# Kernel optimization log

Hardware: AMD Instinct MI355X
Metric: run time of the kernel (lower is better)

The kernel has to match this reference:

```python
import jax, jax.numpy as jnp
import numpy as np

EPS = 1e-7
B, N, DIM, NH, HD, WIN, HASH_WIN = 2, 1024, 512, 8, 64, 64, 8


def expmap0(v, c):
    sqrt_c = jnp.clip(jnp.sqrt(c), EPS)
    v_norm = jnp.linalg.norm(v, axis=-1, keepdims=True)
    is_zero = v_norm < EPS
    safe = jnp.clip(v_norm, EPS)
    mag = jnp.tanh(sqrt_c * safe) / sqrt_c
    return jnp.where(is_zero, jnp.zeros_like(v), mag * (v / safe))


def poincare_dist(x, y, c):
    # x: (B,H,N,1,D), y: (B,H,N,W,D), c: (B,1,1,1,1) -> (B,H,N,W)
    sqrt_c = jnp.clip(jnp.sqrt(c), EPS)
    x2 = jnp.sum(x * x, -1, keepdims=True)
    y2 = jnp.sum(y * y, -1, keepdims=True)
    xy = jnp.sum(x * y, -1, keepdims=True)
    num = (1 - 2 * c * xy + c * y2) * x + (1 - c * x2) * (-y)
    den = 1 - 2 * c * xy + c * c * x2 * y2
    diff = num / jnp.clip(den, EPS)
    dn = jnp.linalg.norm(diff, axis=-1)
    arg = jnp.minimum(jnp.squeeze(sqrt_c, -1) * jnp.clip(dn, EPS), 1.0 - EPS)
    return 2.0 * jnp.arctanh(arg) / jnp.squeeze(sqrt_c, -1)


def sliding_windows(t, w):
    # t: (B,H,N,D) -> (B,H,N,w,D), left-padded causal window
    Bb, H, Nn, D = t.shape
    pad = jnp.zeros((Bb, H, w - 1, D), t.dtype)
    tp = jnp.concatenate([pad, t], axis=2)
    idx = jnp.arange(w)[None, :] + jnp.arange(Nn)[:, None]  # (N,w)
    return tp[:, :, idx, :]


def layernorm(x, s, b):
    m = jnp.mean(x, -1, keepdims=True)
    v = jnp.var(x, -1, keepdims=True)
    return (x - m) / jnp.sqrt(v + 1e-6) * s + b


def rope(x, cos, sin):
    # x: (B,N,H,hd), cos/sin: (N, hd//2) -- complex rotation in real arithmetic
    xr, xi = jnp.split(x, 2, axis=-1)
    cos = cos[None, :, None, :]
    sin = sin[None, :, None, :]
    return jnp.concatenate([xr * cos - xi * sin, xr * sin + xi * cos], axis=-1)


def setup_inputs() -> dict:
    key = jax.random.key(0)
    ks = jax.random.split(key, 10)
    x = jax.random.normal(ks[0], (B, N, DIM), jnp.float32)
    pos = jnp.arange(N, dtype=jnp.float32)
    inv = 1.0 / (10000.0 ** (jnp.arange(0, HD, 2, dtype=jnp.float32) / HD))
    ang = pos[:, None] * inv[None, :]  # (N, HD//2)
    freqs_cos, freqs_sin = jnp.cos(ang), jnp.sin(ang)
    c = jax.random.uniform(ks[1], (B,), jnp.float32) * 0.9 + 0.1
    s = 0.02
    Wq = jax.random.normal(ks[2], (DIM, DIM), jnp.float32) * s
    Wk = jax.random.normal(ks[3], (DIM, DIM), jnp.float32) * s
    Wv = jax.random.normal(ks[4], (DIM, DIM), jnp.float32) * s
    Wo = jax.random.normal(ks[5], (DIM, DIM), jnp.float32) * s
    W1 = jax.random.normal(ks[6], (DIM, 4 * DIM), jnp.float32) * s
    W2 = jax.random.normal(ks[7], (4 * DIM, DIM), jnp.float32) * s
    bq = jnp.zeros((DIM,)); bk = jnp.zeros((DIM,)); bv = jnp.zeros((DIM,))
    bo = jnp.zeros((DIM,)); b1 = jnp.zeros((4 * DIM,)); b2 = jnp.zeros((DIM,))
    ln1_s = jnp.ones((DIM,)); ln1_b = jnp.zeros((DIM,))
    ln2_s = jnp.ones((DIM,)); ln2_b = jnp.zeros((DIM,))
    geo_scale = jnp.ones((NH, 1, 1), jnp.float32)
    hash_offset = jax.random.normal(ks[8], (1, 1, NH, HD), jnp.float32) * 0.01
    return dict(x=x, freqs_cos=freqs_cos, freqs_sin=freqs_sin, c=c,
                Wq=Wq, bq=bq, Wk=Wk, bk=bk, Wv=Wv, bv=bv, Wo=Wo, bo=bo,
                W1=W1, b1=b1, W2=W2, b2=b2,
                ln1_s=ln1_s, ln1_b=ln1_b, ln2_s=ln2_s, ln2_b=ln2_b,
                geo_scale=geo_scale, hash_offset=hash_offset)


def reference(x, freqs_cos, freqs_sin, c, Wq, bq, Wk, bk, Wv, bv, Wo, bo,
              W1, b1, W2, b2, ln1_s, ln1_b, ln2_s, ln2_b, geo_scale, hash_offset):
    x_res = x
    xn = layernorm(x, ln1_s, ln1_b)
    q = (xn @ Wq + bq).reshape(B, N, NH, HD)
    k = (xn @ Wk + bk).reshape(B, N, NH, HD)
    v = (xn @ Wv + bv).reshape(B, N, NH, HD)
    q = q + hash_offset * jnp.log(1.0 + HASH_WIN)
    q_rot = rope(q, freqs_cos, freqs_sin)
    k_rot = rope(k, freqs_cos, freqs_sin)
    c_b = c.reshape(B, 1, 1, 1)
    q_h = expmap0(q_rot, c_b)
    k_h = expmap0(k_rot, c_b)
    q_h, k_h, v = (t.transpose(0, 2, 1, 3) for t in (q_h, k_h, v))  # (B,H,N,D)
    k_win = sliding_windows(k_h, WIN)  # (B,H,N,W,D)
    v_win = sliding_windows(v, WIN)
    dist = poincare_dist(q_h[:, :, :, None, :], k_win, c.reshape(B, 1, 1, 1, 1))  # (B,H,N,W)
    scores = -geo_scale * dist
    w = jax.nn.softmax(scores, axis=-1)
    attn = jnp.einsum('bhnw,bhnwd->bhnd', w, v_win)
    attn = attn.transpose(0, 2, 1, 3).reshape(B, N, DIM)
    x_out = x_res + (attn @ Wo + bo)
    h = layernorm(x_out, ln2_s, ln2_b)
    ffn = jax.nn.gelu(h @ W1 + b1) @ W2 + b2
    return x_out + ffn
```

## Files before the change

### kernel.cpp

```cpp
#include <hip/hip_runtime.h>
#include <math.h>
#include <stdint.h>

#define Bn   2
#define Nn   1024
#define DIMn 512
#define NHn  8
#define HDn  64
#define QKVS 1536
#define EPSF 1e-7f

typedef __attribute__((ext_vector_type(8))) short short8;
typedef __attribute__((ext_vector_type(4))) float floatx4;
typedef __attribute__((ext_vector_type(4))) float fx4;
typedef __attribute__((ext_vector_type(4))) unsigned short usx4;

__device__ __forceinline__ unsigned short f2bf(float f) {
  union { float f; uint32_t u; } v; v.f = f;
  uint32_t u = v.u;
  return (unsigned short)((u + 0x7FFFu + ((u >> 16) & 1u)) >> 16);
}
__device__ __forceinline__ float bf2f(unsigned short h) {
  union { uint32_t u; float f; } v; v.u = ((uint32_t)h) << 16;
  return v.f;
}

__device__ __forceinline__ float wsum(float v) {
#pragma unroll
  for (int m = 32; m >= 1; m >>= 1) v += __shfl_xor(v, m, 64);
  return v;
}

__device__ __forceinline__ float gelu_tanh(float x) {
  const float k0 = 0.7978845608028654f;
  float x3 = x * x * x;
  return 0.5f * x * (1.f + tanhf(k0 * (x + 0.044715f * x3)));
}

__device__ __forceinline__ void glds16(const unsigned short* g, unsigned short* l) {
  __builtin_amdgcn_global_load_lds((const __attribute__((address_space(1))) void*)g,
                                   (__attribute__((address_space(3))) void*)l, 16, 0, 0);
}

__device__ void tr64(const float* __restrict__ W, unsigned short* __restrict__ hi,
                     unsigned short* __restrict__ lo, int K, int N, int tix, int tid,
                     float* tile ) {
  int ntn = N >> 6;
  int kt = tix / ntn, nt = tix - kt * ntn;
  int k0 = kt * 64, n0 = nt * 64;
  int rb = tid >> 4, c4 = (tid & 15) * 4;
#pragma unroll
  for (int rr = 0; rr < 4; ++rr) {
    int r = rr * 16 + rb;
    fx4 v = *(const fx4*)&W[(size_t)(k0 + r) * N + n0 + c4];
    tile[r * 65 + c4] = v.x;
    tile[r * 65 + c4 + 1] = v.y;
    tile[r * 65 + c4 + 2] = v.z;
    tile[r * 65 + c4 + 3] = v.w;
  }
  __syncthreads();
#pragma unroll
  for (int rr = 0; rr < 4; ++rr) {
    int r = rr * 16 + rb;
    usx4 hv, lv;
#pragma unroll
    for (int j = 0; j < 4; ++j) {
      float v = tile[(c4 + j) * 65 + r];
      unsigned short h = f2bf(v);
      hv[j] = h;
      lv[j] = f2bf(v - bf2f(h));
    }
    size_t oi = (size_t)(n0 + r) * K + k0 + c4;
    *(usx4*)&hi[oi] = hv;
    if (lo) *(usx4*)&lo[oi] = lv;
  }
  __syncthreads();
}

__global__ __launch_bounds__(256) void prep_kernel(
    const float* __restrict__ Wq, const float* __restrict__ Wk,
    const float* __restrict__ Wv,
    unsigned short* __restrict__ Wcat_hi, unsigned short* __restrict__ Wcat_lo,
    const float* __restrict__ bq, const float* __restrict__ bk,
    const float* __restrict__ bv, float* __restrict__ bias_cat,
    const float* __restrict__ x, const float* __restrict__ ln1s,
    const float* __restrict__ ln1b,
    unsigned short* __restrict__ xn_hi, unsigned short* __restrict__ xn_lo) {
  __shared__ float tile[64 * 65];
  __shared__ float red[2][4];
  int bid = blockIdx.x;
  int tid = threadIdx.x;
  if (bid < 64) {
    tr64(Wq, Wcat_hi, Wcat_lo, 512, 512, bid, tid, tile);
    return;
  }
  if (bid < 128) {
    tr64(Wk, Wcat_hi + 512 * 512, Wcat_lo + 512 * 512, 512, 512, bid - 64, tid, tile);
    return;
  }
  if (bid < 192) {
    tr64(Wv, Wcat_hi + 1024 * 512, nullptr, 512, 512, bid - 128, tid, tile);
    return;
  }
  if (bid == 192) {
    for (int i = tid; i < 512; i += 256) {
      bias_cat[i] = bq[i];
      bias_cat[512 + i] = bk[i];
      bias_cat[1024 + i] = bv[i];
    }
    return;
  }
  int row = bid - 193;
  const float* xr = x + (size_t)row * DIMn;
  float2 xv = *(const float2*)(xr + tid * 2);
  float s  = xv.x + xv.y;
  float s2 = xv.x * xv.x + xv.y * xv.y;
  s = wsum(s); s2 = wsum(s2);
  int wv = tid >> 6;
  if ((tid & 63) == 0) { red[0][wv] = s; red[1][wv] = s2; }
  __syncthreads();
  s  = red[0][0] + red[0][1] + red[0][2] + red[0][3];
  s2 = red[1][0] + red[1][1] + red[1][2] + red[1][3];
  float mean = s * (1.f / DIMn);
  float var  = s2 * (1.f / DIMn) - mean * mean;
  float rstd = rsqrtf(var + 1e-6f);
  int d = tid * 2;
  float2 gv = *(const float2*)(ln1s + d);
  float2 bv2 = *(const float2*)(ln1b + d);
  float o0 = (xv.x - mean) * rstd * gv.x + bv2.x;
  float o1 = (xv.y - mean) * rstd * gv.y + bv2.y;
  size_t idx = (size_t)row * DIMn + d;
  unsigned short h0 = f2bf(o0), h1 = f2bf(o1);
  ushort2 hv; hv.x = h0; hv.y = h1;
  *(ushort2*)(xn_hi + idx) = hv;
  ushort2 lv; lv.x = f2bf(o0 - bf2f(h0)); lv.y = f2bf(o1 - bf2f(h1));
  *(ushort2*)(xn_lo + idx) = lv;
}

__global__ __launch_bounds__(256) void ln_kernel(const float* __restrict__ x,
                                                 const float* __restrict__ g,
                                                 const float* __restrict__ be,
                                                 unsigned short* __restrict__ yhi) {
  __shared__ float red[2][4];
  int row = blockIdx.x;
  int tid = threadIdx.x;
  const float* xr = x + (size_t)row * DIMn;
  float2 xv = *(const float2*)(xr + tid * 2);
  float s  = xv.x + xv.y;
  float s2 = xv.x * xv.x + xv.y * xv.y;
  s = wsum(s); s2 = wsum(s2);
  int wv = tid >> 6;
  if ((tid & 63) == 0) { red[0][wv] = s; red[1][wv] = s2; }
  __syncthreads();
  s  = red[0][0] + red[0][1] + red[0][2] + red[0][3];
  s2 = red[1][0] + red[1][1] + red[1][2] + red[1][3];
  float mean = s * (1.f / DIMn);
  float var  = s2 * (1.f / DIMn) - mean * mean;
  float rstd = rsqrtf(var + 1e-6f);
  int d = tid * 2;
  float2 gv = *(const float2*)(g + d);
  float2 bv = *(const float2*)(be + d);
  float o0 = (xv.x - mean) * rstd * gv.x + bv.x;
  float o1 = (xv.y - mean) * rstd * gv.y + bv.y;
  size_t idx = (size_t)row * DIMn + d;
  ushort2 hv; hv.x = f2bf(o0); hv.y = f2bf(o1);
  *(ushort2*)(yhi + idx) = hv;
}

template <int BM, int BN, int BKT, int EPI, int OUTBF16>
__global__ __launch_bounds__(256) void gemm_db(
    const unsigned short* __restrict__ Ahi,
    const unsigned short* __restrict__ Bhi,
    const float* __restrict__ bias, const float* __restrict__ res,
    void* __restrict__ outp, int M, int N, int K) {
  constexpr int FI = BM / 32, FJ = BN / 32;
  constexpr int AE = BM * BKT, BE = BN * BKT;
  constexpr int CPR = BKT / 8;
  constexpr int ACH = BM * CPR, BCH = BN * CPR;
  constexpr int CST = BN + 4;
  constexpr int STG = AE + BE;
  constexpr int SMEM_EPI = BM * CST * 2;
  constexpr int SMEM_N = (2 * STG > SMEM_EPI) ? 2 * STG : SMEM_EPI;
  __shared__ __align__(16) unsigned short smem[SMEM_N];

  int tid = threadIdx.x;
  int lane = tid & 63;
  int wid = tid >> 6;
  int wm = (wid >> 1) * (BM / 2), wn = (wid & 1) * (BN / 2);
  int bm = blockIdx.y * BM, bn = blockIdx.x * BN;
  int m16 = lane & 15, kg = lane >> 4;

  floatx4 acc[FI][FJ];
#pragma unroll
  for (int i = 0; i < FI; ++i)
#pragma unroll
    for (int j = 0; j < FJ; ++j) { floatx4 z = {0.f, 0.f, 0.f, 0.f}; acc[i][j] = z; }

  const unsigned short* aph = Ahi + (size_t)bm * K;
  const unsigned short* bph = Bhi + (size_t)bn * K;

  auto stage = [&](int k0, unsigned short* As, unsigned short* Bs) {
    for (int c = tid; c < ACH; c += 256) {
      int row = c / CPR, ci = c % CPR;
      int sci = ci ^ (row & 7);
      glds16(aph + (size_t)row * K + k0 + sci * 8, As + c * 8);
    }
    for (int c = tid; c < BCH; c += 256) {
      int row = c / CPR, ci = c % CPR;
      int sci = ci ^ (row & 7);
      glds16(bph + (size_t)row * K + k0 + sci * 8, Bs + c * 8);
    }
  };

  const int NT = K / BKT;
  stage(0, smem, smem + AE);
  __syncthreads();
  int cur = 0;
  for (int t = 0; t < NT; ++t) {
    unsigned short* As = smem + cur * STG;
    unsigned short* Bs = As + AE;
    int nxt = cur ^ 1;
    if (t + 1 < NT) stage((t + 1) * BKT, smem + nxt * STG, smem + nxt * STG + AE);
#pragma unroll
    for (int ks = 0; ks < BKT / 32; ++ks) {
      short8 ah[FI], bh[FJ];
#pragma unroll
      for (int i = 0; i < FI; ++i) {
        int r = wm + i * 16 + m16;
        ah[i] = *(const short8*)&As[r * BKT + (((ks * 4 + kg) ^ (r & 7)) << 3)];
      }
#pragma unroll
      for (int j = 0; j < FJ; ++j) {
        int r = wn + j * 16 + m16;
        bh[j] = *(const short8*)&Bs[r * BKT + (((ks * 4 + kg) ^ (r & 7)) << 3)];
      }
#pragma unroll
      for (int i = 0; i < FI; ++i)
#pragma unroll
        for (int j = 0; j < FJ; ++j)
          acc[i][j] = __builtin_amdgcn_mfma_f32_16x16x32_bf16(ah[i], bh[j], acc[i][j], 0, 0, 0);
    }
    __syncthreads();
    cur = nxt;
  }

  float* Cs = (float*)smem;
#pragma unroll
  for (int i = 0; i < FI; ++i)
#pragma unroll
    for (int j = 0; j < FJ; ++j)
#pragma unroll
      for (int r = 0; r < 4; ++r)
        Cs[(wm + i * 16 + kg * 4 + r) * CST + wn + j * 16 + m16] = acc[i][j][r];
  __syncthreads();
  constexpr int TOT = BM * BN / 4;
  for (int t = tid; t < TOT; t += 256) {
    int row = (t << 2) / BN;
    int col = (t << 2) & (BN - 1);
    fx4 v = *(const fx4*)&Cs[row * CST + col];
    fx4 bs = *(const fx4*)&bias[bn + col];
    v = v + bs;
    size_t gidx = (size_t)(bm + row) * N + bn + col;
    if constexpr (EPI == 1) {
      fx4 rr = *(const fx4*)&res[gidx];
      v = v + rr;
    }
    if constexpr (EPI == 2) {
      v.x = gelu_tanh(v.x); v.y = gelu_tanh(v.y);
      v.z = gelu_tanh(v.z); v.w = gelu_tanh(v.w);
    }
    if constexpr (OUTBF16) {
      usx4 h;
      h.x = f2bf(v.x); h.y = f2bf(v.y); h.z = f2bf(v.z); h.w = f2bf(v.w);
      *(usx4*)((unsigned short*)outp + gidx) = h;
    } else {
      *(fx4*)((float*)outp + gidx) = v;
    }
  }
}

__global__ __launch_bounds__(256) void qkv_gemm(
    const unsigned short* __restrict__ Ahi, const unsigned short* __restrict__ Alo,
    const unsigned short* __restrict__ Bhi, const unsigned short* __restrict__ Blo,
    const float* __restrict__ bias, float* __restrict__ outp,
    const float* __restrict__ Wo, const float* __restrict__ W1,
    const float* __restrict__ W2,
    unsigned short* __restrict__ Wo_t, unsigned short* __restrict__ W1_t,
    unsigned short* __restrict__ W2_t) {
  constexpr int BM = 64, BN = 64, BKT = 32, K = 512, N = QKVS;
  constexpr int FI = 2, FJ = 2;
  constexpr int AE = BM * BKT, BE = BN * BKT;
  constexpr int CST = BN + 4;
  constexpr int STG = 2 * (AE + BE);
  constexpr int SMEM_EPI = BM * CST * 2;
  constexpr int SMEM_N = (2 * STG > SMEM_EPI) ? 2 * STG : SMEM_EPI;
  __shared__ __align__(16) unsigned short smem[SMEM_N];

  int tid = threadIdx.x;
  int bid = blockIdx.x;

  if (bid >= 768) {
    float* tile = (float*)smem;
    int tix = bid - 768;
    if (tix < 64)       tr64(Wo, Wo_t, nullptr, 512, 512, tix, tid, tile);
    else if (tix < 320) tr64(W1, W1_t, nullptr, 512, 2048, tix - 64, tid, tile);
    else                tr64(W2, W2_t, nullptr, 2048, 512, tix - 320, tid, tile);
    return;
  }

  int lane = tid & 63;
  int wid = tid >> 6;
  int wm = (wid >> 1) * 32, wn = (wid & 1) * 32;
  int bm = (bid / 24) * BM, bn = (bid % 24) * BN;
  int m16 = lane & 15, kg = lane >> 4;
  bool dos = bn < 1024;

  floatx4 acc[FI][FJ];
#pragma unroll
  for (int i = 0; i < FI; ++i)
#pragma unroll
    for (int j = 0; j < FJ; ++j) { floatx4 z = {0.f, 0.f, 0.f, 0.f}; acc[i][j] = z; }

  const unsigned short* aph = Ahi + (size_t)bm * K;
  const unsigned short* bph = Bhi + (size_t)bn * K;
  const unsigned short* apl = Alo + (size_t)bm * K;
  const unsigned short* bpl = Blo + (size_t)bn * K;

  auto stage = [&](int k0, unsigned short* buf) {
    {
      int c = tid;
      int row = c >> 2, ci = c & 3;
      int sci = ci ^ ((row >> 1) & 3);
      glds16(aph + (size_t)row * K + k0 + sci * 8, buf + c * 8);
      if (dos) glds16(apl + (size_t)row * K + k0 + sci * 8, buf + AE + c * 8);
    }
    {
      int c = tid;
      int row = c >> 2, ci = c & 3;
      int sci = ci ^ ((row >> 1) & 3);
      glds16(bph + (size_t)row * K + k0 + sci * 8, buf + 2 * AE + c * 8);
      if (dos) glds16(bpl + (size_t)row * K + k0 + sci * 8, buf + 2 * AE + BE + c * 8);
    }
  };

  const int NT = K / BKT;
  stage(0, smem);
  __syncthreads();
  int cur = 0;
  for (int t = 0; t < NT; ++t) {
    unsigned short* buf = smem + cur * STG;
    unsigned short* AsHi = buf;
    unsigned short* AsLo = buf + AE;
    unsigned short* BsHi = buf + 2 * AE;
    unsigned short* BsLo = buf + 2 * AE + BE;
    int nxt = cur ^ 1;
    if (t + 1 < NT) stage((t + 1) * BKT, smem + nxt * STG);

    short8 ah[FI], bh[FJ], al[FI], bl[FJ];
#pragma unroll
    for (int i = 0; i < FI; ++i) {
      int r = wm + i * 16 + m16;
      int off = r * BKT + ((kg ^ ((r >> 1) & 3)) << 3);
      ah[i] = *(const short8*)&AsHi[off];
      if (dos) al[i] = *(const short8*)&AsLo[off];
    }
#pragma unroll
    for (int j = 0; j < FJ; ++j) {
      int r = wn + j * 16 + m16;
      int off = r * BKT + ((kg ^ ((r >> 1) & 3)) << 3);
      bh[j] = *(const short8*)&BsHi[off];
      if (dos) bl[j] = *(const short8*)&BsLo[off];
    }
#pragma unroll
    for (int i = 0; i < FI; ++i)
#pragma unroll
      for (int j = 0; j < FJ; ++j) {
        acc[i][j] = __builtin_amdgcn_mfma_f32_16x16x32_bf16(ah[i], bh[j], acc[i][j], 0, 0, 0);
        if (dos) {
          acc[i][j] = __builtin_amdgcn_mfma_f32_16x16x32_bf16(al[i], bh[j], acc[i][j], 0, 0, 0);
          acc[i][j] = __builtin_amdgcn_mfma_f32_16x16x32_bf16(ah[i], bl[j], acc[i][j], 0, 0, 0);
        }
      }
    __syncthreads();
    cur = nxt;
  }

  float* Cs = (float*)smem;
#pragma unroll
  for (int i = 0; i < FI; ++i)
#pragma unroll
    for (int j = 0; j < FJ; ++j)
#pragma unroll
      for (int r = 0; r < 4; ++r)
        Cs[(wm + i * 16 + kg * 4 + r) * CST + wn + j * 16 + m16] = acc[i][j][r];
  __syncthreads();
  constexpr int TOT = BM * BN / 4;
  for (int t = tid; t < TOT; t += 256) {
    int row = (t << 2) / BN;
    int col = (t << 2) & (BN - 1);
    fx4 v = *(const fx4*)&Cs[row * CST + col];
    fx4 bs = *(const fx4*)&bias[bn + col];
    v = v + bs;
    size_t gidx = (size_t)(bm + row) * N + bn + col;
    *(fx4*)(outp + gidx) = v;
  }
}

__global__ __launch_bounds__(512) void attn_fused(const float* __restrict__ qkv,
                                                  const float* __restrict__ fcos,
                                                  const float* __restrict__ fsin,
                                                  const float* __restrict__ cvec,
                                                  const float* __restrict__ geo,
                                                  const float* __restrict__ hash,
                                                  unsigned short* __restrict__ attn_out) {
  __shared__ unsigned short Qhi[32][72], Qlo[32][72];
  __shared__ unsigned short Khi[96][72], Klo[96][72];
  __shared__ unsigned short Vt[64][104];
  __shared__ unsigned short Pb[32][104];
  __shared__ float Sf[32][97];
  __shared__ float x2s[32], bxs[32], y2s[96], gys[96];

  int tid = threadIdx.x, lane = tid & 63, wv = tid >> 6;
  int bid = blockIdx.x;
  int nt = bid & 31, h = (bid >> 5) & 7, b = bid >> 8;
  int n0 = nt * 32;
  float c = cvec[b];
  float sqc = sqrtf(c);
  float rsqc = 1.f / sqc;
  float gs = geo[h];
  int dr = lane & 31;
  bool hih = lane >= 32;
  const float LOG9 = 2.1972245773362196f;
  float hofr = hash[h * HDn + dr] * LOG9;
  float hofi = hash[h * HDn + dr + 32] * LOG9;

  for (int i = tid; i < 32 * 52; i += 512) ((uint32_t*)Pb)[i] = 0u;

#pragma unroll
  for (int i = 0; i < 4; ++i) {
    int q = wv * 4 + i;
    int n = n0 + q;
    size_t bas = (size_t)(b * Nn + n) * QKVS + h * HDn;
    float qr = qkv[bas + dr] + hofr;
    float qi = qkv[bas + dr + 32] + hofi;
    float cs = fcos[n * 32 + dr], sn = fsin[n * 32 + dr];
    float qv = hih ? (qr * sn + qi * cs) : (qr * cs - qi * sn);
    float nq = sqrtf(wsum(qv * qv));
    float sq = fmaxf(nq, EPSF);
    float t = sqc * sq;
    float em = expf(-2.f * t);
    float opem = 1.f + em;
    float mag = ((1.f - em) / opem) * rsqc;
    float sech2 = 4.f * em / (opem * opem);
    float oq = (nq < EPSF) ? 0.f : mag * (qv / sq);
    unsigned short hh = f2bf(oq);
    Qhi[q][lane] = hh;
    Qlo[q][lane] = f2bf(oq - bf2f(hh));
    if (lane == 0) {
      x2s[q] = (nq < EPSF) ? 0.f : mag * mag;
      bxs[q] = (nq < EPSF) ? 1.f : sech2;
    }
  }
#pragma unroll 4
  for (int i = 0; i < 12; ++i) {
    int r = wv * 12 + i;
    int gi = n0 - 64 + r;
    float ok = 0.f, vf = 0.f, y2 = 0.f, gy = 1.f;
    if (gi >= 0) {
      size_t bas = (size_t)(b * Nn + gi) * QKVS + h * HDn;
      float kr = qkv[bas + 512 + dr];
      float ki = qkv[bas + 512 + dr + 32];
      vf = qkv[bas + 1024 + lane];
      float cs = fcos[gi * 32 + dr], sn = fsin[gi * 32 + dr];
      float kv = hih ? (kr * sn + ki * cs) : (kr * cs - ki * sn);
      float nk = sqrtf(wsum(kv * kv));
      float sk = fmaxf(nk, EPSF);
      float t = sqc * sk;
      float em = expf(-2.f * t);
      float opem = 1.f + em;
      float mag = ((1.f - em) / opem) * rsqc;
      float sech2 = 4.f * em / (opem * opem);
      ok = (nk < EPSF) ? 0.f : mag * (kv / sk);
      y2 = (nk < EPSF) ? 0.f : mag * mag;
      gy = (nk < EPSF) ? 1.f : sech2;
    }
    unsigned short hh = f2bf(ok);
    Khi[r][lane] = hh;
    Klo[r][lane] = f2bf(ok - bf2f(hh));
    Vt[lane][r] = f2bf(vf);
    if (lane == 0) { y2s[r] = y2; gys[r] = gy; }
  }
  __syncthreads();

  int m16 = lane & 15, kg = lane >> 4;
#pragma unroll
  for (int uu = 0; uu < 2; ++uu) {
    int u = wv + uu * 8;
    if (u < 12) {
      int mt = u / 6, ntile = u % 6;
      floatx4 acc = {0.f, 0.f, 0.f, 0.f};
#pragma unroll
      for (int ks = 0; ks < 2; ++ks) {
        short8 ah = *(const short8*)&Qhi[mt * 16 + m16][ks * 32 + kg * 8];
        short8 al = *(const short8*)&Qlo[mt * 16 + m16][ks * 32 + kg * 8];
        short8 bh = *(const short8*)&Khi[ntile * 16 + m16][ks * 32 + kg * 8];
        short8 bl = *(const short8*)&Klo[ntile * 16 + m16][ks * 32 + kg * 8];
        acc = __builtin_amdgcn_mfma_f32_16x16x32_bf16(ah, bh, acc, 0, 0, 0);
        acc = __builtin_amdgcn_mfma_f32_16x16x32_bf16(al, bh, acc, 0, 0, 0);
        acc = __builtin_amdgcn_mfma_f32_16x16x32_bf16(ah, bl, acc, 0, 0, 0);
      }
#pragma unroll
      for (int r = 0; r < 4; ++r) Sf[mt * 16 + kg * 4 + r][ntile * 16 + m16] = acc[r];
    }
  }
  __syncthreads();

#pragma unroll
  for (int i = 0; i < 4; ++i) {
    int nl = wv * 4 + i;
    int r = nl + 1 + lane;
    float xy = Sf[nl][r];
    float x2 = x2s[nl], y2 = y2s[r];
    float bx = bxs[nl], gy = gys[r];

    float den = fmaf(c * c * x2, y2, fmaf(-2.f * c, xy, 1.f));
    den = fmaxf(den, EPSF);
    float rden = 1.f / den;
    float s2 = fmaxf(x2 - 2.f * xy + y2, 0.f);
    float z = sqrtf(c * s2 * rden);
    float omz2 = bx * gy * rden;
    float opz = 1.f + fminf(z, 1.f);
    float ratio = fminf(opz * opz / omz2, 1.9999999e7f);
    float sc = -gs * logf(ratio) * rsqc;

    float e = expf(sc);
    float se = wsum(e);
    Pb[nl][r] = f2bf(e / se);
  }
  __syncthreads();

  {
    int mt = wv >> 2, ntile = wv & 3;
    floatx4 acc = {0.f, 0.f, 0.f, 0.f};
#pragma unroll
    for (int ks = 0; ks < 3; ++ks) {
      short8 a = *(const short8*)&Pb[mt * 16 + m16][ks * 32 + kg * 8];
      short8 bb = *(const short8*)&Vt[ntile * 16 + m16][ks * 32 + kg * 8];
      acc = __builtin_amdgcn_mfma_f32_16x16x32_bf16(a, bb, acc, 0, 0, 0);
    }
#pragma unroll
    for (int r = 0; r < 4; ++r) {
      int qrow = mt * 16 + kg * 4 + r;
      int d = ntile * 16 + m16;
      attn_out[(size_t)(b * Nn + n0 + qrow) * DIMn + h * HDn + d] = f2bf(acc[r]);
    }
  }
}

extern "C" void kernel_launch(void* const* d_in, const int* in_sizes, int n_in,
                              void* d_out, int out_size, void* d_ws, size_t ws_size,
                              hipStream_t stream) {
  const float* x    = (const float*)d_in[0];
  const float* fcos = (const float*)d_in[1];
  const float* fsin = (const float*)d_in[2];
  const float* cvec = (const float*)d_in[3];
  const float* Wq = (const float*)d_in[4];  const float* bq = (const float*)d_in[5];
  const float* Wk = (const float*)d_in[6];  const float* bk = (const float*)d_in[7];
  const float* Wv = (const float*)d_in[8];  const float* bv = (const float*)d_in[9];
  const float* Wo = (const float*)d_in[10]; const float* bo = (const float*)d_in[11];
  const float* W1 = (const float*)d_in[12]; const float* b1 = (const float*)d_in[13];
  const float* W2 = (const float*)d_in[14]; const float* b2 = (const float*)d_in[15];
  const float* ln1s = (const float*)d_in[16]; const float* ln1b = (const float*)d_in[17];
  const float* ln2s = (const float*)d_in[18]; const float* ln2b = (const float*)d_in[19];
  const float* geo  = (const float*)d_in[20]; const float* hash = (const float*)d_in[21];
  float* out = (float*)d_out;
  char* base = (char*)d_ws;

  unsigned short* Wcat_hi = (unsigned short*)(base + 0);
  unsigned short* Wcat_lo = (unsigned short*)(base + 1572864);
  unsigned short* Wo_t    = (unsigned short*)(base + 3145728);
  unsigned short* W1_t    = (unsigned short*)(base + 3670016);
  unsigned short* W2_t    = (unsigned short*)(base + 5767168);
  unsigned short* xn_hi   = (unsigned short*)(base + 7864320);
  unsigned short* xn_lo   = (unsigned short*)(base + 9961472);
  float*          qkv     = (float*)(base + 12058624);
  unsigned short* attnb   = (unsigned short*)(base + 7864320);
  float*          xout    = (float*)(base + 9961472);
  unsigned short* hbuf    = (unsigned short*)(base + 14155776);
  unsigned short* mid     = (unsigned short*)(base + 16252928);
  float*          bias_cat= (float*)(base + 24641536);

  const int M = Bn * Nn;

  prep_kernel<<<193 + M, 256, 0, stream>>>(Wq, Wk, Wv, Wcat_hi, Wcat_lo,
                                           bq, bk, bv, bias_cat,
                                           x, ln1s, ln1b, xn_hi, xn_lo);
  qkv_gemm<<<768 + 576, 256, 0, stream>>>(
      xn_hi, xn_lo, Wcat_hi, Wcat_lo, bias_cat, qkv,
      Wo, W1, W2, Wo_t, W1_t, W2_t);
  attn_fused<<<Bn * NHn * (Nn / 32), 512, 0, stream>>>(qkv, fcos, fsin, cvec, geo, hash, attnb);
  gemm_db<32, 32, 64, 1, 0><<<dim3(DIMn / 32, M / 32), 256, 0, stream>>>(
      attnb, Wo_t, bo, x, xout, M, DIMn, 512);
  ln_kernel<<<M, 256, 0, stream>>>(xout, ln2s, ln2b, hbuf);
  gemm_db<64, 64, 64, 2, 1><<<dim3(2048 / 64, M / 64), 256, 0, stream>>>(
      hbuf, W1_t, b1, nullptr, mid, M, 2048, 512);
  gemm_db<32, 32, 64, 1, 0><<<dim3(DIMn / 32, M / 32), 256, 0, stream>>>(
      mid, W2_t, b2, xout, out, M, DIMn, 2048);
}
```

Before: 179.9 us.

## Precompute hyperbolic Q/K transform in separate kernel to avoid redundant window recomputation

Moves the RoPE, hash offset, expmap0 and bf16 hi/lo split of Q and K, plus the V bf16 conversion, into a new per-token kernel that writes to workspace buffers. The attention kernel then only loads the precomputed bf16 tiles and auxiliary norms. This removes the 3x recomputation of the K transform caused by overlapping 96-row windows per 32-query tile. In exchange it adds a kernel launch and an extra global write/read round trip of the transformed tensors.

```diff
diff --git a/kernel.cpp b/kernel.cpp
--- a/kernel.cpp
+++ b/kernel.cpp
@@ -406,44 +406,31 @@
   }
 }
 
-__global__ __launch_bounds__(512) void attn_fused(const float* __restrict__ qkv,
-                                                  const float* __restrict__ fcos,
-                                                  const float* __restrict__ fsin,
-                                                  const float* __restrict__ cvec,
-                                                  const float* __restrict__ geo,
-                                                  const float* __restrict__ hash,
-                                                  unsigned short* __restrict__ attn_out) {
-  __shared__ unsigned short Qhi[32][72], Qlo[32][72];
-  __shared__ unsigned short Khi[96][72], Klo[96][72];
-  __shared__ unsigned short Vt[64][104];
-  __shared__ unsigned short Pb[32][104];
-  __shared__ float Sf[32][97];
-  __shared__ float x2s[32], bxs[32], y2s[96], gys[96];
-
-  int tid = threadIdx.x, lane = tid & 63, wv = tid >> 6;
-  int bid = blockIdx.x;
-  int nt = bid & 31, h = (bid >> 5) & 7, b = bid >> 8;
-  int n0 = nt * 32;
+__global__ __launch_bounds__(512) void qk_transform(
+    const float* __restrict__ qkv, const float* __restrict__ fcos,
+    const float* __restrict__ fsin, const float* __restrict__ cvec,
+    const float* __restrict__ hash,
+    unsigned short* __restrict__ qh_hi, unsigned short* __restrict__ qh_lo,
+    unsigned short* __restrict__ kh_hi, unsigned short* __restrict__ kh_lo,
+    unsigned short* __restrict__ vb, float2* __restrict__ qaux,
+    float2* __restrict__ kaux) {
+  int tid = threadIdx.x, lane = tid & 63, h = tid >> 6;
+  int token = blockIdx.x;
+  int b = token >> 10, n = token & 1023;
   float c = cvec[b];
-  float sqc = sqrtf(c);
-  float rsqc = 1.f / sqc;
-  float gs = geo[h];
+  float sqc = sqrtf(c), rsqc = 1.f / sqc;
   int dr = lane & 31;
   bool hih = lane >= 32;
   const float LOG9 = 2.1972245773362196f;
-  float hofr = hash[h * HDn + dr] * LOG9;
-  float hofi = hash[h * HDn + dr + 32] * LOG9;
-
-  for (int i = tid; i < 32 * 52; i += 512) ((uint32_t*)Pb)[i] = 0u;
-
-#pragma unroll
-  for (int i = 0; i < 4; ++i) {
-    int q = wv * 4 + i;
-    int n = n0 + q;
-    size_t bas = (size_t)(b * Nn + n) * QKVS + h * HDn;
-    float qr = qkv[bas + dr] + hofr;
-    float qi = qkv[bas + dr + 32] + hofi;
-    float cs = fcos[n * 32 + dr], sn = fsin[n * 32 + dr];
+  float cs = fcos[n * 32 + dr], sn = fsin[n * 32 + dr];
+  size_t bas = (size_t)token * QKVS + h * HDn;
+  size_t ob = (size_t)token * DIMn + h * HDn;
+
+  vb[ob + lane] = f2bf(qkv[bas + 1024 + lane]);
+
+  {
+    float qr = qkv[bas + dr] + hash[h * HDn + dr] * LOG9;
+    float qi = qkv[bas + dr + 32] + hash[h * HDn + dr + 32] * LOG9;
     float qv = hih ? (qr * sn + qi * cs) : (qr * cs - qi * sn);
     float nq = sqrtf(wsum(qv * qv));
     float sq = fmaxf(nq, EPSF);
@@ -454,41 +441,92 @@
     float sech2 = 4.f * em / (opem * opem);
     float oq = (nq < EPSF) ? 0.f : mag * (qv / sq);
     unsigned short hh = f2bf(oq);
-    Qhi[q][lane] = hh;
-    Qlo[q][lane] = f2bf(oq - bf2f(hh));
+    qh_hi[ob + lane] = hh;
+    qh_lo[ob + lane] = f2bf(oq - bf2f(hh));
     if (lane == 0) {
-      x2s[q] = (nq < EPSF) ? 0.f : mag * mag;
-      bxs[q] = (nq < EPSF) ? 1.f : sech2;
+      float2 a;
+      a.x = (nq < EPSF) ? 0.f : mag * mag;
+      a.y = (nq < EPSF) ? 1.f : sech2;
+      qaux[(size_t)token * NHn + h] = a;
+    }
+  }
+  {
+    float kr = qkv[bas + 512 + dr];
+    float ki = qkv[bas + 512 + dr + 32];
+    float kv = hih ? (kr * sn + ki * cs) : (kr * cs - ki * sn);
+    float nk = sqrtf(wsum(kv * kv));
+    float sk = fmaxf(nk, EPSF);
+    float t = sqc * sk;
+    float em = expf(-2.f * t);
+    float opem = 1.f + em;
+    float mag = ((1.f - em) / opem) * rsqc;
+    float sech2 = 4.f * em / (opem * opem);
+    float ok = (nk < EPSF) ? 0.f : mag * (kv / sk);
+    unsigned short hh = f2bf(ok);
+    kh_hi[ob + lane] = hh;
+    kh_lo[ob + lane] = f2bf(ok - bf2f(hh));
+    if (lane == 0) {
+      float2 a;
+      a.x = (nk < EPSF) ? 0.f : mag * mag;
+      a.y = (nk < EPSF) ? 1.f : sech2;
+      kaux[(size_t)token * NHn + h] = a;
+    }
+  }
+}
+
+__global__ __launch_bounds__(512) void attn_fused(
+    const unsigned short* __restrict__ qh_hi, const unsigned short* __restrict__ qh_lo,
+    const unsigned short* __restrict__ kh_hi, const unsigned short* __restrict__ kh_lo,
+    const unsigned short* __restrict__ vb, const float2* __restrict__ qaux,
+    const float2* __restrict__ kaux, const float* __restrict__ cvec,
+    const float* __restrict__ geo, unsigned short* __restrict__ attn_out) {
+  __shared__ unsigned short Qhi[32][72], Qlo[32][72];
+  __shared__ unsigned short Khi[96][72], Klo[96][72];
+  __shared__ unsigned short Vt[64][104];
+  __shared__ unsigned short Pb[32][104];
+  __shared__ float Sf[32][97];
+  __shared__ float x2s[32], bxs[32], y2s[96], gys[96];
+
+  int tid = threadIdx.x, lane = tid & 63, wv = tid >> 6;
+  int bid = blockIdx.x;
+  int nt = bid & 31, h = (bid >> 5) & 7, b = bid >> 8;
+  int n0 = nt * 32;
+  float c = cvec[b];
+  float sqc = sqrtf(c);
+  float rsqc = 1.f / sqc;
+  float gs = geo[h];
+
+  for (int i = tid; i < 32 * 52; i += 512) ((uint32_t*)Pb)[i] = 0u;
+
+#pragma unroll
+  for (int i = 0; i < 4; ++i) {
+    int q = wv * 4 + i;
+    int n = n0 + q;
+    size_t bas = (size_t)(b * Nn + n) * DIMn + h * HDn;
+    Qhi[q][lane] = qh_hi[bas + lane];
+    Qlo[q][lane] = qh_lo[bas + lane];
+    if (lane == 0) {
+      float2 a = qaux[(size_t)(b * Nn + n) * NHn + h];
+      x2s[q] = a.x; bxs[q] = a.y;
     }
   }
 #pragma unroll 4
   for (int i = 0; i < 12; ++i) {
     int r = wv * 12 + i;
     int gi = n0 - 64 + r;
-    float ok = 0.f, vf = 0.f, y2 = 0.f, gy = 1.f;
     if (gi >= 0) {
-      size_t bas = (size_t)(b * Nn + gi) * QKVS + h * HDn;
-      float kr = qkv[bas + 512 + dr];
-      float ki = qkv[bas + 512 + dr + 32];
-      vf = qkv[bas + 1024 + lane];
-      float cs = fcos[gi * 32 + dr], sn = fsin[gi * 32 + dr];
-      float kv = hih ? (kr * sn + ki * cs) : (kr * cs - ki * sn);
-      float nk = sqrtf(wsum(kv * kv));
-      float sk = fmaxf(nk, EPSF);
-      float t = sqc * sk;
-      float em = expf(-2.f * t);
-      float opem = 1.f + em;
-      float mag = ((1.f - em) / opem) * rsqc;
-      float sech2 = 4.f * em / (opem * opem);
-      ok = (nk < EPSF) ? 0.f : mag * (kv / sk);
-      y2 = (nk < EPSF) ? 0.f : mag * mag;
-      gy = (nk < EPSF) ? 1.f : sech2;
-    }
-    unsigned short hh = f2bf(ok);
-    Khi[r][lane] = hh;
-    Klo[r][lane] = f2bf(ok - bf2f(hh));
-    Vt[lane][r] = f2bf(vf);
-    if (lane == 0) { y2s[r] = y2; gys[r] = gy; }
+      size_t bas = (size_t)(b * Nn + gi) * DIMn + h * HDn;
+      Khi[r][lane] = kh_hi[bas + lane];
+      Klo[r][lane] = kh_lo[bas + lane];
+      Vt[lane][r] = vb[bas + lane];
+      if (lane == 0) {
+        float2 a = kaux[(size_t)(b * Nn + gi) * NHn + h];
+        y2s[r] = a.x; gys[r] = a.y;
+      }
+    } else {
+      Khi[r][lane] = 0; Klo[r][lane] = 0; Vt[lane][r] = 0;
+      if (lane == 0) { y2s[r] = 0.f; gys[r] = 1.f; }
+    }
   }
   __syncthreads();
 
@@ -589,6 +627,13 @@
   unsigned short* hbuf    = (unsigned short*)(base + 14155776);
   unsigned short* mid     = (unsigned short*)(base + 16252928);
   float*          bias_cat= (float*)(base + 24641536);
+  unsigned short* qh_hi   = (unsigned short*)(base + 25165824);
+  unsigned short* qh_lo   = (unsigned short*)(base + 27262976);
+  unsigned short* kh_hi   = (unsigned short*)(base + 29360128);
+  unsigned short* kh_lo   = (unsigned short*)(base + 31457280);
+  unsigned short* vbuf    = (unsigned short*)(base + 33554432);
+  float2*         qaux    = (float2*)(base + 35651584);
+  float2*         kaux    = (float2*)(base + 35782656);
 
   const int M = Bn * Nn;
 
@@ -598,7 +643,10 @@
   qkv_gemm<<<768 + 576, 256, 0, stream>>>(
       xn_hi, xn_lo, Wcat_hi, Wcat_lo, bias_cat, qkv,
       Wo, W1, W2, Wo_t, W1_t, W2_t);
-  attn_fused<<<Bn * NHn * (Nn / 32), 512, 0, stream>>>(qkv, fcos, fsin, cvec, geo, hash, attnb);
+  qk_transform<<<M, 512, 0, stream>>>(qkv, fcos, fsin, cvec, hash,
+                                      qh_hi, qh_lo, kh_hi, kh_lo, vbuf, qaux, kaux);
+  attn_fused<<<Bn * NHn * (Nn / 32), 512, 0, stream>>>(
+      qh_hi, qh_lo, kh_hi, kh_lo, vbuf, qaux, kaux, cvec, geo, attnb);
   gemm_db<32, 32, 64, 1, 0><<<dim3(DIMn / 32, M / 32), 256, 0, stream>>>(
       attnb, Wo_t, bo, x, xout, M, DIMn, 512);
   ln_kernel<<<M, 256, 0, stream>>>(xout, ln2s, ln2b, hbuf);
```

After: 183.6 us. 2.1% more time.
